# Kernel optimization log

Measured on AMD Instinct MI355X. Metric: run time of the kernel, lower is better.

The kernel has to match this reference:

```python
import jax, jax.numpy as jnp
import numpy as np

KERNEL_SIZE = 3  # matches init kwarg

def setup_inputs() -> dict:
    key = jax.random.key(0)
    k1, k2, k3, k4 = jax.random.split(key, 4)
    N, C, L, OUT = 32, 64, 2048, 128
    inp = jax.random.normal(k1, (N, C, L), dtype=jnp.float32)
    # adjacency-like dense matrix (tree adjacency may be sparse; dense here)
    m = jax.random.uniform(k2, (N, L, L), dtype=jnp.float32)
    W = jax.random.normal(k3, (OUT, KERNEL_SIZE * C), dtype=jnp.float32) * 0.05
    b = jax.random.normal(k4, (OUT,), dtype=jnp.float32)
    return {"input": inp, "m": m, "W": W, "b": b}

def reference(input, m, W, b):
    # propagate features over the tree adjacency kernel_size-1 times
    ys = [input]
    y = input
    for _ in range(KERNEL_SIZE - 1):
        y = jnp.matmul(y, m)          # (N, C, L) @ (N, L, L) -> (N, C, L)
        ys.append(y)
    cat = jnp.concatenate(ys, axis=1)  # (N, k*C, L)
    # 1x1 conv == channel projection
    out = jnp.einsum('oc,ncl->nol', W, cat) + b[None, :, None]
    return out
```

## Files before the change

kernel.cpp:

```cpp
#include <hip/hip_runtime.h>
#include <hip/hip_bf16.h>

#define NB   32
#define CH   64
#define LL   2048
#define OUTC 128

typedef float  f32x4  __attribute__((ext_vector_type(4)));
typedef short  s16x8  __attribute__((ext_vector_type(8)));
typedef short  s16x4  __attribute__((ext_vector_type(4)));
typedef unsigned short u16;

__device__ __forceinline__ u16 f2bf(float f) {
  unsigned int u = __builtin_bit_cast(unsigned int, f);
  u += 0x7FFFu + ((u >> 16) & 1u);
  return (u16)(u >> 16);
}

__device__ __forceinline__ s16x8 pack8c(const float* v) {
  s16x8 r;
#pragma unroll
  for (int j = 0; j < 8; j += 2) {
    __hip_bfloat162 h = __float22bfloat162_rn(make_float2(v[j], v[j + 1]));
    short2 s;
    __builtin_memcpy(&s, &h, sizeof(s));
    r[j] = s.x; r[j + 1] = s.y;
  }
  return r;
}

__device__ __forceinline__ s16x4 pack4c(const f32x4& v) {
  s16x4 r;
  __hip_bfloat162 h0 = __float22bfloat162_rn(make_float2(v[0], v[1]));
  __hip_bfloat162 h1 = __float22bfloat162_rn(make_float2(v[2], v[3]));
  short2 s0, s1;
  __builtin_memcpy(&s0, &h0, sizeof(s0));
  __builtin_memcpy(&s1, &h1, sizeof(s1));
  r[0] = s0.x; r[1] = s0.y; r[2] = s1.x; r[3] = s1.y;
  return r;
}

#define NX (NB * CH * LL)
#define NW (OUTC * 3 * CH)
__global__ __launch_bounds__(256)
void cvt_inputs(const float* __restrict__ x, const float* __restrict__ W,
                u16* __restrict__ xb, u16* __restrict__ Wb)
{
  const size_t t8 = ((size_t)blockIdx.x * 256 + threadIdx.x) * 8;
  if (t8 < NX) {
    float v[8];
    *(f32x4*)(v)     = *(const f32x4*)(x + t8);
    *(f32x4*)(v + 4) = *(const f32x4*)(x + t8 + 4);
    *(s16x8*)(xb + t8) = pack8c(v);
  } else if (t8 - NX < NW) {
    const size_t w8 = t8 - NX;
    float v[8];
    *(f32x4*)(v)     = *(const f32x4*)(W + w8);
    *(f32x4*)(v + 4) = *(const f32x4*)(W + w8 + 4);
    *(s16x8*)(Wb + w8) = pack8c(v);
  }
}

__global__ __launch_bounds__(256, 2)
void prop1_pack(const u16* __restrict__ xb, const float* __restrict__ m,
                u16* __restrict__ y1, u16* __restrict__ mP)
{
  __shared__ float smem[3][32 * 128];

  const int n    = blockIdx.x >> 4;
  const int lt   = blockIdx.x & 15;
  const int tid  = threadIdx.x;
  const int wave = tid >> 6;
  const int lane = tid & 63;
  const int l15  = lane & 15;
  const int g4   = lane >> 4;
  const int colb = lt * 128 + wave * 32;

  const float* mn = m + (size_t)n * LL * LL + lt * 128;
  const float* gsrc = mn + (size_t)(wave * 8 + (lane >> 5)) * LL + (lane & 31) * 4;

  const u16* ap = xb + (size_t)n * CH * LL + (size_t)l15 * LL + g4 * 8;
  u16* q0 = mP + (((size_t)n * 64 * LL + colb + l15) * 4 + g4) * 8;
  u16* o  = y1 + (size_t)n * CH * LL + colb + l15;

  f32x4 acc[4][2];
#pragma unroll
  for (int f = 0; f < 4; ++f)
#pragma unroll
    for (int h = 0; h < 2; ++h)
#pragma unroll
      for (int r = 0; r < 4; ++r) acc[f][h][r] = 0.f;

#define GLOAD(SB, KB)                                                         \
  { float* _sb = (SB);                                                        \
    _Pragma("unroll") for (int i = 0; i < 4; ++i) {                           \
      const float* _g = gsrc + (size_t)((KB) * 32 + i * 2) * LL;              \
      __builtin_amdgcn_global_load_lds(                                       \
        (const __attribute__((address_space(1))) void*)_g,                    \
        (__attribute__((address_space(3))) void*)(_sb + (wave * 4 + i) * 256),\
        16, 0, 0); } }

  GLOAD(smem[0], 0)
  GLOAD(smem[1], 1)
  asm volatile("s_waitcnt vmcnt(4)" ::: "memory");
  __builtin_amdgcn_s_barrier();
  __builtin_amdgcn_sched_barrier(0);

  int bc = 0;
#pragma unroll 1
  for (int kb = 0; kb < 64; ++kb) {
    s16x8 a[4];
    const u16* a_ = ap + kb * 32;
#pragma unroll
    for (int f = 0; f < 4; ++f) a[f] = *(const s16x8*)(a_ + (size_t)(f * 16) * LL);
    __builtin_amdgcn_sched_barrier(0);

    const int b2 = (bc == 0) ? 2 : bc - 1;
    if (kb + 2 < 64) GLOAD(smem[b2], kb + 2)

    const float* t = smem[bc] + wave * 32 + l15;
    float bv0[8], bv1[8];
#pragma unroll
    for (int j = 0; j < 8; ++j) {
      bv0[j] = t[(g4 * 8 + j) * 128];
      bv1[j] = t[(g4 * 8 + j) * 128 + 16];
    }
    s16x8 b0 = pack8c(bv0), b1 = pack8c(bv1);

    u16* q = q0 + (size_t)kb * 65536;
    *(s16x8*)(q)       = b0;
    *(s16x8*)(q + 512) = b1;

#pragma unroll
    for (int f = 0; f < 4; ++f) {
      acc[f][0] = __builtin_amdgcn_mfma_f32_16x16x32_bf16(a[f], b0, acc[f][0], 0, 0, 0);
      acc[f][1] = __builtin_amdgcn_mfma_f32_16x16x32_bf16(a[f], b1, acc[f][1], 0, 0, 0);
    }

    if (kb + 1 < 64) {
      asm volatile("s_waitcnt vmcnt(6)" ::: "memory");
      __builtin_amdgcn_s_barrier();
      __builtin_amdgcn_sched_barrier(0);
    }
    bc = (bc == 2) ? 0 : bc + 1;
  }

#pragma unroll
  for (int f = 0; f < 4; ++f)
#pragma unroll
    for (int r = 0; r < 4; ++r) {
      const int row = f * 16 + g4 * 4 + r;
      o[(size_t)row * LL]      = f2bf(acc[f][0][r]);
      o[(size_t)row * LL + 16] = f2bf(acc[f][1][r]);
    }
}

__global__ __launch_bounds__(256, 2)
void prop2_proj(const u16* __restrict__ y1, const u16* __restrict__ mP,
                const u16* __restrict__ xb, const u16* __restrict__ Wb,
                const float* __restrict__ bias, float* __restrict__ out)
{
  __shared__ u16 yT[128 * 72];

  const int n    = blockIdx.x >> 4;
  const int lt   = blockIdx.x & 15;
  const int tid  = threadIdx.x;
  const int wave = tid >> 6;
  const int lane = tid & 63;
  const int l15  = lane & 15;
  const int g4   = lane >> 4;
  const int colb = lt * 128 + wave * 32;

  const u16* mq = mP + (((size_t)n * 64 * LL + colb + l15) * 4 + g4) * 8;
  const u16* ap = y1 + (size_t)n * CH * LL + (size_t)l15 * LL + g4 * 8;

  f32x4 acc[4][2];
#pragma unroll
  for (int f = 0; f < 4; ++f)
#pragma unroll
    for (int h = 0; h < 2; ++h)
#pragma unroll
      for (int r = 0; r < 4; ++r) acc[f][h][r] = 0.f;

  s16x8 bA0, bA1, bB0, bB1, aA[4], aB[4];

#define K2_LOAD(B0, B1, AV, KB)                                              \
  {                                                                          \
    const u16* _mq = mq + (size_t)(KB) * 65536;                              \
    B0 = *(const s16x8*)(_mq);                                               \
    B1 = *(const s16x8*)(_mq + 512);                                         \
    const u16* _ap = ap + (KB) * 32;                                         \
    _Pragma("unroll") for (int f = 0; f < 4; ++f)                            \
      AV[f] = *(const s16x8*)(_ap + (size_t)(f * 16) * LL);                  \
  }

#define K2_COMP(B0, B1, AV)                                                  \
  _Pragma("unroll") for (int f = 0; f < 4; ++f) {                            \
    acc[f][0] = __builtin_amdgcn_mfma_f32_16x16x32_bf16(AV[f], B0, acc[f][0], 0, 0, 0); \
    acc[f][1] = __builtin_amdgcn_mfma_f32_16x16x32_bf16(AV[f], B1, acc[f][1], 0, 0, 0); \
  }

  K2_LOAD(bA0, bA1, aA, 0)
#pragma unroll 1
  for (int kb = 0; kb < 64; kb += 2) {
    K2_LOAD(bB0, bB1, aB, kb + 1)
    K2_COMP(bA0, bA1, aA)
    if (kb + 2 < 64) K2_LOAD(bA0, bA1, aA, kb + 2)
    K2_COMP(bB0, bB1, aB)
  }

#pragma unroll
  for (int f = 0; f < 4; ++f)
#pragma unroll
    for (int h = 0; h < 2; ++h) {
      const int c = wave * 32 + l15 + 16 * h;
      *(s16x4*)(&yT[c * 72 + f * 16 + g4 * 4]) = pack4c(acc[f][h]);
    }
  __syncthreads();

  f32x4 acc2[8][2];
#pragma unroll
  for (int f = 0; f < 8; ++f)
#pragma unroll
    for (int h = 0; h < 2; ++h)
#pragma unroll
      for (int r = 0; r < 4; ++r) acc2[f][h][r] = 0.f;

  const size_t cb = (size_t)n * CH * LL + colb + l15;
  const u16* xp  = xb + cb + (size_t)(g4 * 8) * LL;
  const u16* y1p = y1 + cb + (size_t)(g4 * 8) * LL;
  const u16* wq  = Wb + (size_t)l15 * 192 + g4 * 8;

#pragma unroll
  for (int kc = 0; kc < 6; ++kc) {
    const int k0 = kc * 32;
    s16x8 b0, b1;
    if (kc < 4) {
      const u16* src = (kc < 2) ? (xp + (size_t)k0 * LL)
                                : (y1p + (size_t)(k0 - 64) * LL);
#pragma unroll
      for (int j = 0; j < 8; ++j) {
        b0[j] = (short)src[(size_t)j * LL];
        b1[j] = (short)src[(size_t)j * LL + 16];
      }
    } else {
      const int rb = (kc - 4) * 32 + g4 * 8;
      b0 = *(const s16x8*)(&yT[(wave * 32 + l15) * 72 + rb]);
      b1 = *(const s16x8*)(&yT[(wave * 32 + l15 + 16) * 72 + rb]);
    }
#pragma unroll
    for (int f = 0; f < 8; ++f) {
      s16x8 af = *(const s16x8*)(wq + (size_t)(f * 16) * 192 + k0);
      acc2[f][0] = __builtin_amdgcn_mfma_f32_16x16x32_bf16(af, b0, acc2[f][0], 0, 0, 0);
      acc2[f][1] = __builtin_amdgcn_mfma_f32_16x16x32_bf16(af, b1, acc2[f][1], 0, 0, 0);
    }
  }

  float* op = out + (size_t)n * OUTC * LL + colb + l15;
#pragma unroll
  for (int f = 0; f < 8; ++f)
#pragma unroll
    for (int r = 0; r < 4; ++r) {
      const int row = f * 16 + g4 * 4 + r;
      op[(size_t)row * LL]      = acc2[f][0][r] + bias[row];
      op[(size_t)row * LL + 16] = acc2[f][1][r] + bias[row];
    }
}

extern "C" void kernel_launch(void* const* d_in, const int* in_sizes, int n_in,
                              void* d_out, int out_size, void* d_ws, size_t ws_size,
                              hipStream_t stream)
{
  const float* x = (const float*)d_in[0];
  const float* m = (const float*)d_in[1];
  const float* W = (const float*)d_in[2];
  const float* b = (const float*)d_in[3];
  float* out = (float*)d_out;

  u16* y1 = (u16*)d_ws;
  u16* xb = y1 + (size_t)NB * CH * LL;
  u16* Wb = xb + (size_t)NB * CH * LL;
  u16* mP = (u16*)((char*)d_ws + (25u << 20));

  cvt_inputs<<<dim3(2060), dim3(256), 0, stream>>>(x, W, xb, Wb);
  prop1_pack<<<dim3(NB * 16), dim3(256), 0, stream>>>(xb, m, y1, mP);
  prop2_proj<<<dim3(NB * 16), dim3(256), 0, stream>>>(y1, mP, xb, Wb, b, out);
}
```

Measured before the change: 279.6 us.

## Deepen prop1 pipeline to four LDS stages and double-buffer A fragments

The prop1_pack kernel moves from a 3-stage to a 4-stage LDS ring for m tiles and prefetches the next iteration's xb A-fragments into alternating register sets. The loop is unrolled by two with explicit vmcnt waits tuned to the in-flight load counts. The aim is to hide global-load latency for both operands behind the MFMA work. In exchange it uses more LDS (64KB per block), which may cut occupancy from two blocks per CU, and the hand-counted waitcnts are fragile.

```diff
diff --git a/kernel.cpp b/kernel.cpp
--- a/kernel.cpp
+++ b/kernel.cpp
@@ -65,7 +65,7 @@
 void prop1_pack(const u16* __restrict__ xb, const float* __restrict__ m,
                 u16* __restrict__ y1, u16* __restrict__ mP)
 {
-  __shared__ float smem[3][32 * 128];
+  __shared__ float smem[4][32 * 128];
 
   const int n    = blockIdx.x >> 4;
   const int lt   = blockIdx.x & 15;
@@ -76,10 +76,9 @@
   const int g4   = lane >> 4;
   const int colb = lt * 128 + wave * 32;
 
-  const float* mn = m + (size_t)n * LL * LL + lt * 128;
+  const float* mn   = m + (size_t)n * LL * LL + lt * 128;
   const float* gsrc = mn + (size_t)(wave * 8 + (lane >> 5)) * LL + (lane & 31) * 4;
-
-  const u16* ap = xb + (size_t)n * CH * LL + (size_t)l15 * LL + g4 * 8;
+  const u16*   ap   = xb + (size_t)n * CH * LL + (size_t)l15 * LL + g4 * 8;
   u16* q0 = mP + (((size_t)n * 64 * LL + colb + l15) * 4 + g4) * 8;
   u16* o  = y1 + (size_t)n * CH * LL + colb + l15;
 
@@ -91,8 +90,15 @@
 #pragma unroll
       for (int r = 0; r < 4; ++r) acc[f][h][r] = 0.f;
 
-#define GLOAD(SB, KB)                                                         \
-  { float* _sb = (SB);                                                        \
+  s16x8 aP[4], aQ[4];
+
+#define ALOAD(R, KB)                                                          \
+  { const u16* _ap = ap + (KB) * 32;                                          \
+    _Pragma("unroll") for (int f = 0; f < 4; ++f)                             \
+      R[f] = *(const s16x8*)(_ap + (size_t)(f * 16) * LL); }
+
+#define GLOAD(BI, KB)                                                         \
+  { float* _sb = smem[BI];                                                    \
     _Pragma("unroll") for (int i = 0; i < 4; ++i) {                           \
       const float* _g = gsrc + (size_t)((KB) * 32 + i * 2) * LL;              \
       __builtin_amdgcn_global_load_lds(                                       \
@@ -100,50 +106,53 @@
         (__attribute__((address_space(3))) void*)(_sb + (wave * 4 + i) * 256),\
         16, 0, 0); } }
 
-  GLOAD(smem[0], 0)
-  GLOAD(smem[1], 1)
-  asm volatile("s_waitcnt vmcnt(4)" ::: "memory");
+  ALOAD(aP, 0)
+  __builtin_amdgcn_sched_barrier(0);
+  GLOAD(0, 0) GLOAD(1, 1) GLOAD(2, 2)
+  __builtin_amdgcn_sched_barrier(0);
+  asm volatile("s_waitcnt vmcnt(8)" ::: "memory");
   __builtin_amdgcn_s_barrier();
   __builtin_amdgcn_sched_barrier(0);
 
-  int bc = 0;
+#define K1_STEP(KB, CUR, NXT, VN, LAST)                                       \
+  {                                                                           \
+    if (!(LAST)) {                                                            \
+      ALOAD(NXT, ((KB) + 1 < 64 ? (KB) + 1 : 63))                             \
+      __builtin_amdgcn_sched_barrier(0);                                      \
+      GLOAD(((KB) + 3) & 3, ((KB) + 3 < 64 ? (KB) + 3 : 63))                  \
+      __builtin_amdgcn_sched_barrier(0);                                      \
+    }                                                                         \
+    const float* _t = smem[(KB) & 3] + wave * 32 + l15;                       \
+    float _bv0[8], _bv1[8];                                                   \
+    _Pragma("unroll") for (int j = 0; j < 8; ++j) {                           \
+      _bv0[j] = _t[(g4 * 8 + j) * 128];                                       \
+      _bv1[j] = _t[(g4 * 8 + j) * 128 + 16];                                  \
+    }                                                                         \
+    s16x8 _b0 = pack8c(_bv0), _b1 = pack8c(_bv1);                             \
+    u16* _q = q0 + (size_t)(KB) * 65536;                                      \
+    *(s16x8*)(_q)       = _b0;                                                \
+    *(s16x8*)(_q + 512) = _b1;                                                \
+    _Pragma("unroll") for (int f = 0; f < 4; ++f) {                           \
+      acc[f][0] = __builtin_amdgcn_mfma_f32_16x16x32_bf16(CUR[f], _b0, acc[f][0], 0, 0, 0); \
+      acc[f][1] = __builtin_amdgcn_mfma_f32_16x16x32_bf16(CUR[f], _b1, acc[f][1], 0, 0, 0); \
+    }                                                                         \
+    if (!(LAST)) {                                                            \
+      __builtin_amdgcn_sched_barrier(0);                                      \
+      asm volatile("s_waitcnt vmcnt(" VN ")" ::: "memory");                   \
+      __builtin_amdgcn_s_barrier();                                           \
+      __builtin_amdgcn_sched_barrier(0);                                      \
+    }                                                                         \
+  }
+
+  K1_STEP(0, aP, aQ, "14", false)
+  K1_STEP(1, aQ, aP, "20", false)
 #pragma unroll 1
-  for (int kb = 0; kb < 64; ++kb) {
-    s16x8 a[4];
-    const u16* a_ = ap + kb * 32;
-#pragma unroll
-    for (int f = 0; f < 4; ++f) a[f] = *(const s16x8*)(a_ + (size_t)(f * 16) * LL);
-    __builtin_amdgcn_sched_barrier(0);
-
-    const int b2 = (bc == 0) ? 2 : bc - 1;
-    if (kb + 2 < 64) GLOAD(smem[b2], kb + 2)
-
-    const float* t = smem[bc] + wave * 32 + l15;
-    float bv0[8], bv1[8];
-#pragma unroll
-    for (int j = 0; j < 8; ++j) {
-      bv0[j] = t[(g4 * 8 + j) * 128];
-      bv1[j] = t[(g4 * 8 + j) * 128 + 16];
-    }
-    s16x8 b0 = pack8c(bv0), b1 = pack8c(bv1);
-
-    u16* q = q0 + (size_t)kb * 65536;
-    *(s16x8*)(q)       = b0;
-    *(s16x8*)(q + 512) = b1;
-
-#pragma unroll
-    for (int f = 0; f < 4; ++f) {
-      acc[f][0] = __builtin_amdgcn_mfma_f32_16x16x32_bf16(a[f], b0, acc[f][0], 0, 0, 0);
-      acc[f][1] = __builtin_amdgcn_mfma_f32_16x16x32_bf16(a[f], b1, acc[f][1], 0, 0, 0);
-    }
-
-    if (kb + 1 < 64) {
-      asm volatile("s_waitcnt vmcnt(6)" ::: "memory");
-      __builtin_amdgcn_s_barrier();
-      __builtin_amdgcn_sched_barrier(0);
-    }
-    bc = (bc == 2) ? 0 : bc + 1;
-  }
+  for (int kb = 2; kb < 62; kb += 2) {
+    K1_STEP(kb,     aP, aQ, "22", false)
+    K1_STEP(kb + 1, aQ, aP, "22", false)
+  }
+  K1_STEP(62, aP, aQ, "22", false)
+  K1_STEP(63, aQ, aP, "0",  true)
 
 #pragma unroll
   for (int f = 0; f < 4; ++f)
```

Measured after the change: 271.6 us (median of 2 runs). -2.8%, faster.
